# Kernel tuning notes

Measured on AMD Instinct MI355X. Metric: run time of the kernel, lower is better.

## Reference

```python
import jax, jax.numpy as jnp
import numpy as np

NEG = -1e30  # finite stand-in for -inf so logsumexp grads stay finite


def ctc_loss_mean(y_true, log_probs_tm, input_length, label_length, blank=0):
    """CTC loss (forward algorithm in log space), mean over batch.

    log_probs_tm: [T, B, C] time-major log-probabilities.
    y_true:       [B, L] dense int labels (blank=0 excluded from real labels).
    """
    T, B, C = log_probs_tm.shape
    L = y_true.shape[1]
    S = 2 * L + 1  # extended label length: blank, l1, blank, l2, ...
    ll = jnp.clip(label_length, 1, L)
    il = jnp.clip(input_length, 1, T)

    # Extended label sequence: blanks at even positions, labels at odd.
    ext = jnp.full((B, S), blank, dtype=jnp.int32).at[:, 1::2].set(y_true.astype(jnp.int32))
    ext_m2 = jnp.concatenate([jnp.full((B, 2), -1, jnp.int32), ext[:, :-2]], axis=1)
    # Skip transition (s-2 -> s) allowed only for label positions with no repeat.
    allow_skip = ((jnp.arange(S) % 2 == 1)[None, :]) & (ext != ext_m2)

    lp0 = jnp.take_along_axis(log_probs_tm[0], ext, axis=1)  # [B, S]
    alpha0 = jnp.full((B, S), NEG, log_probs_tm.dtype)
    alpha0 = alpha0.at[:, 0].set(lp0[:, 0]).at[:, 1].set(lp0[:, 1])

    def step(alpha, xs):
        lp_t, t = xs
        lpe = jnp.take_along_axis(lp_t, ext, axis=1)  # [B, S]
        a1 = jnp.concatenate([jnp.full((B, 1), NEG, alpha.dtype), alpha[:, :-1]], axis=1)
        a2 = jnp.concatenate([jnp.full((B, 2), NEG, alpha.dtype), alpha[:, :-2]], axis=1)
        a2 = jnp.where(allow_skip, a2, NEG)
        new = jax.nn.logsumexp(jnp.stack([alpha, a1, a2]), axis=0) + lpe
        # Freeze alpha once past each example's input_length.
        return jnp.where((t < il)[:, None], new, alpha), None

    alpha, _ = jax.lax.scan(step, alpha0, (log_probs_tm[1:], jnp.arange(1, T)))

    # Loss = -log(alpha[2*ll-1] + alpha[2*ll]) at the final (frozen) time step.
    idx = jnp.stack([2 * ll - 1, 2 * ll], axis=1)  # [B, 2]
    end_vals = jnp.take_along_axis(alpha, idx, axis=1)
    loss = -jax.nn.logsumexp(end_vals, axis=1)
    return jnp.mean(loss)


def setup_inputs() -> dict:
    key = jax.random.key(0)
    kx, kl, ki, kj = jax.random.split(key, 4)
    B, T, C, L = 64, 1024, 128, 256
    # y_pred are probabilities (module applies log), so softmax random logits.
    y_pred = jax.nn.softmax(jax.random.normal(kx, (B, T, C), jnp.float32), axis=-1)
    y_true = jax.random.randint(kl, (B, L), 1, C, jnp.int32)  # blank=0 excluded
    input_length = jax.random.randint(ki, (B,), T // 2, T + 1, jnp.int32)
    label_length = jax.random.randint(kj, (B,), L // 2, L + 1, jnp.int32)
    return {"y_true": y_true, "y_pred": y_pred,
            "input_length": input_length, "label_length": label_length}


def reference(y_true, y_pred, input_length, label_length):
    # Mirror CTCLayer.call: log + transpose to time-major, reshape lengths.
    log_tm = jnp.log(jnp.transpose(y_pred, (1, 0, 2)))  # [T, B, C]
    loss = ctc_loss_mean(y_true, log_tm,
                         input_length.reshape(-1), label_length.reshape(-1),
                         blank=0)
    return log_tm, loss
```

## Files before the change

### kernel.cpp

```cpp
#include <hip/hip_runtime.h>
#include <math.h>

constexpr int B = 64;
constexpr int T = 1024;
constexpr int C = 128;
constexpr int L = 256;
constexpr int S = 2 * L + 1;
constexpr int TRB = 2048;

template <int N> struct IC { static constexpr int value = N; };

__device__ __forceinline__ float shr1(float x) {
    return __int_as_float(__builtin_amdgcn_update_dpp(
        0, __float_as_int(x), 0x138 , 0xf, 0xf, false));
}

template <int CTRL>
__device__ __forceinline__ float maxdpp(float x) {
    float t = __int_as_float(__builtin_amdgcn_update_dpp(
        __float_as_int(x), __float_as_int(x), CTRL, 0xf, 0xf, false));
    return fmaxf(x, t);
}

__device__ __forceinline__ float wave_max_dpp(float x) {
    x = maxdpp<0x111>(x);
    x = maxdpp<0x112>(x);
    x = maxdpp<0x114>(x);
    x = maxdpp<0x118>(x);
    x = maxdpp<0x142>(x);
    x = maxdpp<0x143>(x);
    return __int_as_float(__builtin_amdgcn_readlane(__float_as_int(x), 63));
}

__global__
__attribute__((amdgpu_waves_per_eu(1, 1)))
__launch_bounds__(64)
void ctc_fused(
    const float* __restrict__ yp,
    const int*   __restrict__ yt,
    const int*   __restrict__ il_,
    const int*   __restrict__ ll_,
    float* __restrict__ out_log,
    float* __restrict__ out_loss)
{
    const int lane = threadIdx.x;
    if (blockIdx.x >= B) {
        int id = blockIdx.x - B;
        int bb = id >> 5;
        int ck = id & 31;
        const float4* src = (const float4*)yp + ((size_t)bb * T + ck * 32) * 32;
        float4* o4 = (float4*)out_log;
        #pragma unroll
        for (int k = 0; k < 16; ++k) {
            int o = k * 64 + lane;
            float4 v = src[o];
            int tt = ck * 32 + (o >> 5);
            int c4 = o & 31;
            float4 r;
            r.x = __logf(v.x); r.y = __logf(v.y);
            r.z = __logf(v.z); r.w = __logf(v.w);
            o4[((size_t)tt * B + bb) * 32 + c4] = r;
        }
        return;
    }

    const int b = blockIdx.x;

    __shared__ float lsh[2048];
    __shared__ float afin[S];

    int il = il_[b]; il = min(max(il, 1), T);
    int ll = ll_[b]; ll = min(max(ll, 1), L);
    const float* yb = yp + (size_t)b * T * C;

    int4 y4  = *(const int4*)(yt + b * L + 4 * lane);
    int  po  = lane ? 4 * lane - 4 : 0;
    int4 py4 = *(const int4*)(yt + b * L + po);
    int  ppw = yt[b * L + (lane >= 2 ? 4 * lane - 5 : 0)];

    int lab[8]   = {py4.x, py4.y, py4.z, py4.w, y4.x, y4.y, y4.z, y4.w};
    int labm1[8] = {ppw,   py4.x, py4.y, py4.z, py4.w, y4.x, y4.y, y4.z};
    float skf[8];
    #pragma unroll
    for (int k = 0; k < 8; ++k)
        skf[k] = ((4 * lane + k >= 5) && (lab[k] != labm1[k])) ? 1.f : 0.f;

    const int c0 = y4.x, c1 = y4.y, c2 = y4.z, c3 = y4.w;

    auto ldpair = [&](int m) -> float4 {
        int r = 2 * m + 1 + (lane >> 5);
        r = r > T - 1 ? T - 1 : r;
        return ((const float4*)(yb + (size_t)r * C))[lane & 31];
    };

    float p00 = yb[0];
    float p0l = yb[c0];

    float4 q0 = ldpair(0), q1 = ldpair(1);
    float4 q2 = ldpair(2), q3 = ldpair(3);
    float4 prr[8];
    #pragma unroll
    for (int m = 4; m <= 11; ++m) prr[m & 7] = ldpair(m);

    ((float4*)(lsh +   0))[lane] = q0;
    ((float4*)(lsh + 256))[lane] = q1;
    ((float4*)(lsh + 512))[lane] = q2;
    ((float4*)(lsh + 768))[lane] = q3;

    float gv[4][4][4], gbv[4][4];
    #pragma unroll
    for (int q = 0; q < 2; ++q)
        #pragma unroll
        for (int j = 0; j < 4; ++j) {
            const float* base = lsh + q * 512 + j * 128;
            gbv[q][j] = base[0];
            gv[q][j][0] = base[c0]; gv[q][j][1] = base[c1];
            gv[q][j][2] = base[c2]; gv[q][j][3] = base[c3];
        }

    float w[17];
    #pragma unroll
    for (int i = 0; i < 17; ++i) w[i] = 0.f;
    if (lane == 0) { w[8] = p00; w[9] = p0l; }

    auto halo = [&]() {
        #pragma unroll
        for (int k = 0; k < 8; ++k) w[k] = shr1(w[8 + k]);
    };
    halo();

    int lsi = 0;
    int t0 = 0;

    auto group = [&](auto Pc, auto S0c) {
        constexpr int P  = decltype(Pc)::value;
        constexpr int S0 = decltype(S0c)::value;
        constexpr int BF = (P + 2) & 3;
        float g1[4], g2[4], g3[4];
        #pragma unroll
        for (int j = 0; j < 4; ++j) {
            g1[j] = shr1(gv[P][j][1]);
            g2[j] = shr1(gv[P][j][2]);
            g3[j] = shr1(gv[P][j][3]);
        }
        #pragma unroll
        for (int j = 0; j < 4; ++j) {
            #pragma unroll
            for (int i = 16; i >= 2 * (j + 1); --i) {
                float acc = w[i] + w[i - 1];
                float g;
                if (i & 1) {
                    const int k = (i - 1) >> 1;
                    acc = fmaf(skf[k], w[i - 2], acc);
                    g = (k >= 4) ? gv[P][j][k - 4]
                                 : (k == 1 ? g1[j] : (k == 2 ? g2[j] : g3[j]));
                } else {
                    g = gbv[P][j];
                }
                w[i] = acc * g;
            }
        }
        ((float4*)(lsh + BF * 512      ))[lane] = prr[S0];
        ((float4*)(lsh + BF * 512 + 256))[lane] = prr[S0 + 1];
        prr[S0]     = ldpair((t0 >> 1) + 12);
        prr[S0 + 1] = ldpair((t0 >> 1) + 13);
        #pragma unroll
        for (int j = 0; j < 4; ++j) {
            const float* base = lsh + BF * 512 + j * 128;
            gbv[BF][j] = base[0];
            gv[BF][j][0] = base[c0]; gv[BF][j][1] = base[c1];
            gv[BF][j][2] = base[c2]; gv[BF][j][3] = base[c3];
        }
        __builtin_amdgcn_sched_barrier(0x7);
        halo();
        t0 += 4;
    };

    auto maxw = [&]() {
        return fmaxf(fmaxf(fmaxf(w[8], w[9]), fmaxf(w[10], w[11])),
                     fmaxf(fmaxf(w[12], w[13]),
                           fmaxf(fmaxf(w[14], w[15]), w[16])));
    };
    auto rescale = [&]() {
        float mm = wave_max_dpp(maxw());
        int eb = (__float_as_int(mm) >> 23) & 0xff;
        int sh = 350 - eb;
        sh = sh > 254 ? 254 : (sh < 1 ? 1 : sh);
        float inv = __int_as_float(sh << 23);
        #pragma unroll
        for (int i = 8; i < 17; ++i) w[i] *= inv;
        lsi -= sh - 127;
    };

    const int full_end = ((il - 1) >> 2) << 2;

    while (t0 + 16 <= full_end) {
        group(IC<0>{}, IC<4>{});
        group(IC<1>{}, IC<6>{});
        rescale();
        group(IC<2>{}, IC<0>{});
        group(IC<3>{}, IC<2>{});
        rescale();
    }

    if (t0 + 4 <= full_end) { group(IC<0>{}, IC<4>{}); rescale(); }
    if (t0 + 4 <= full_end) { group(IC<1>{}, IC<6>{}); rescale(); }
    if (t0 + 4 <= full_end) { group(IC<2>{}, IC<0>{}); }

    const int ph = (full_end >> 2) & 3;
    float tg[3][4], tb[3];
    switch (ph) {
    case 0:
        #pragma unroll
        for (int j = 0; j < 3; ++j) { tb[j]=gbv[0][j]; tg[j][0]=gv[0][j][0]; tg[j][1]=gv[0][j][1]; tg[j][2]=gv[0][j][2]; tg[j][3]=gv[0][j][3]; }
        break;
    case 1:
        #pragma unroll
        for (int j = 0; j < 3; ++j) { tb[j]=gbv[1][j]; tg[j][0]=gv[1][j][0]; tg[j][1]=gv[1][j][1]; tg[j][2]=gv[1][j][2]; tg[j][3]=gv[1][j][3]; }
        break;
    case 2:
        #pragma unroll
        for (int j = 0; j < 3; ++j) { tb[j]=gbv[2][j]; tg[j][0]=gv[2][j][0]; tg[j][1]=gv[2][j][1]; tg[j][2]=gv[2][j][2]; tg[j][3]=gv[2][j][3]; }
        break;
    default:
        #pragma unroll
        for (int j = 0; j < 3; ++j) { tb[j]=gbv[3][j]; tg[j][0]=gv[3][j][0]; tg[j][1]=gv[3][j][1]; tg[j][2]=gv[3][j][2]; tg[j][3]=gv[3][j][3]; }
        break;
    }
    #pragma unroll
    for (int j = 0; j < 3; ++j) {
        int r = full_end + 1 + j;
        if (r < il) {
            float hh = shr1(w[15]);
            float gb = tb[j];
            float n8  = (w[8] + hh) * gb;
            float n9  = fmaf(skf[4], hh,    w[9]  + w[8])  * tg[j][0];
            float n10 = (w[10] + w[9])  * gb;
            float n11 = fmaf(skf[5], w[9],  w[11] + w[10]) * tg[j][1];
            float n12 = (w[12] + w[11]) * gb;
            float n13 = fmaf(skf[6], w[11], w[13] + w[12]) * tg[j][2];
            float n14 = (w[14] + w[13]) * gb;
            float n15 = fmaf(skf[7], w[13], w[15] + w[14]) * tg[j][3];
            float n16 = (w[16] + w[15]) * gb;
            w[8] = n8;  w[9] = n9;  w[10] = n10; w[11] = n11; w[12] = n12;
            w[13] = n13; w[14] = n14; w[15] = n15; w[16] = n16;
        }
    }

    #pragma unroll
    for (int k = 0; k < 8; ++k) afin[8 * lane + k] = w[8 + k];
    if (lane == 63) afin[512] = w[16];
    __syncthreads();
    if (lane == 0) {
        float e1 = afin[2 * ll - 1];
        float e2 = afin[2 * ll];
        float sum = fmaxf(e1 + e2, 1e-37f);
        float loss = -(__log2f(sum) + (float)lsi) * 0.6931471805599453f;
        atomicAdd(out_loss, loss * (1.0f / (float)B));
    }
}

extern "C" void kernel_launch(void* const* d_in, const int* in_sizes, int n_in,
                              void* d_out, int out_size, void* d_ws, size_t ws_size,
                              hipStream_t stream) {
    const int*   y_true = (const int*)d_in[0];
    const float* y_pred = (const float*)d_in[1];
    const int*   in_len = (const int*)d_in[2];
    const int*   lb_len = (const int*)d_in[3];

    float* out_log  = (float*)d_out;
    float* out_loss = (float*)d_out + (size_t)T * B * C;

    hipMemsetAsync(out_loss, 0, sizeof(float), stream);
    ctc_fused<<<B + TRB, 64, 0, stream>>>(y_pred, y_true, in_len, lb_len,
                                          out_log, out_loss);
}
```

Baseline: 186.7 us.

## Gather emission probabilities directly from global memory and defer rescale application

Removes the LDS staging buffer and the float4 row prefetch; each group now gathers the needed per-label probabilities straight from global memory three groups ahead. The wave-wide max reduction for rescaling is split into a measure step and a later apply step, so the DPP reduction latency overlaps the next group's recurrence instead of stalling it. DPP moves use mov_dpp with bound_ctrl. The cost is scattered global loads, which may expose more latency than the LDS path did.

```diff
diff --git a/kernel.cpp b/kernel.cpp
--- a/kernel.cpp
+++ b/kernel.cpp
@@ -11,14 +11,24 @@
 template <int N> struct IC { static constexpr int value = N; };
 
 __device__ __forceinline__ float shr1(float x) {
+#if __has_builtin(__builtin_amdgcn_mov_dpp)
+    return __int_as_float(__builtin_amdgcn_mov_dpp(
+        __float_as_int(x), 0x138 , 0xf, 0xf, true));
+#else
     return __int_as_float(__builtin_amdgcn_update_dpp(
-        0, __float_as_int(x), 0x138 , 0xf, 0xf, false));
+        0, __float_as_int(x), 0x138, 0xf, 0xf, true));
+#endif
 }
 
 template <int CTRL>
 __device__ __forceinline__ float maxdpp(float x) {
+#if __has_builtin(__builtin_amdgcn_mov_dpp)
+    float t = __int_as_float(__builtin_amdgcn_mov_dpp(
+        __float_as_int(x), CTRL, 0xf, 0xf, true));
+#else
     float t = __int_as_float(__builtin_amdgcn_update_dpp(
-        __float_as_int(x), __float_as_int(x), CTRL, 0xf, 0xf, false));
+        0, __float_as_int(x), CTRL, 0xf, 0xf, true));
+#endif
     return fmaxf(x, t);
 }
 
@@ -66,7 +76,6 @@
 
     const int b = blockIdx.x;
 
-    __shared__ float lsh[2048];
     __shared__ float afin[S];
 
     int il = il_[b]; il = min(max(il, 1), T);
@@ -87,36 +96,31 @@
 
     const int c0 = y4.x, c1 = y4.y, c2 = y4.z, c3 = y4.w;
 
-    auto ldpair = [&](int m) -> float4 {
-        int r = 2 * m + 1 + (lane >> 5);
-        r = r > T - 1 ? T - 1 : r;
-        return ((const float4*)(yb + (size_t)r * C))[lane & 31];
+    int z0;
+    asm volatile("v_mov_b32 %0, 0" : "=v"(z0));
+
+    float gv[4][4][4], gbv[4][4];
+
+    auto fill = [&](auto Qc, int r0) {
+        constexpr int Q = decltype(Qc)::value;
+        #pragma unroll
+        for (int j = 0; j < 4; ++j) {
+            int r = r0 + j; r = r < T ? r : T - 1;
+            const float* rb = yb + (size_t)r * C;
+            gbv[Q][j]   = rb[z0];
+            gv[Q][j][0] = rb[c0];
+            gv[Q][j][1] = rb[c1];
+            gv[Q][j][2] = rb[c2];
+            gv[Q][j][3] = rb[c3];
+        }
     };
 
     float p00 = yb[0];
     float p0l = yb[c0];
 
-    float4 q0 = ldpair(0), q1 = ldpair(1);
-    float4 q2 = ldpair(2), q3 = ldpair(3);
-    float4 prr[8];
-    #pragma unroll
-    for (int m = 4; m <= 11; ++m) prr[m & 7] = ldpair(m);
-
-    ((float4*)(lsh +   0))[lane] = q0;
-    ((float4*)(lsh + 256))[lane] = q1;
-    ((float4*)(lsh + 512))[lane] = q2;
-    ((float4*)(lsh + 768))[lane] = q3;
-
-    float gv[4][4][4], gbv[4][4];
-    #pragma unroll
-    for (int q = 0; q < 2; ++q)
-        #pragma unroll
-        for (int j = 0; j < 4; ++j) {
-            const float* base = lsh + q * 512 + j * 128;
-            gbv[q][j] = base[0];
-            gv[q][j][0] = base[c0]; gv[q][j][1] = base[c1];
-            gv[q][j][2] = base[c2]; gv[q][j][3] = base[c3];
-        }
+    fill(IC<0>{}, 1);
+    fill(IC<1>{}, 5);
+    fill(IC<2>{}, 9);
 
     float w[17];
     #pragma unroll
@@ -132,10 +136,9 @@
     int lsi = 0;
     int t0 = 0;
 
-    auto group = [&](auto Pc, auto S0c) {
-        constexpr int P  = decltype(Pc)::value;
-        constexpr int S0 = decltype(S0c)::value;
-        constexpr int BF = (P + 2) & 3;
+    auto group = [&](auto Pc) {
+        constexpr int P = decltype(Pc)::value;
+        constexpr int F = (P + 3) & 3;
         float g1[4], g2[4], g3[4];
         #pragma unroll
         for (int j = 0; j < 4; ++j) {
@@ -160,17 +163,7 @@
                 w[i] = acc * g;
             }
         }
-        ((float4*)(lsh + BF * 512      ))[lane] = prr[S0];
-        ((float4*)(lsh + BF * 512 + 256))[lane] = prr[S0 + 1];
-        prr[S0]     = ldpair((t0 >> 1) + 12);
-        prr[S0 + 1] = ldpair((t0 >> 1) + 13);
-        #pragma unroll
-        for (int j = 0; j < 4; ++j) {
-            const float* base = lsh + BF * 512 + j * 128;
-            gbv[BF][j] = base[0];
-            gv[BF][j][0] = base[c0]; gv[BF][j][1] = base[c1];
-            gv[BF][j][2] = base[c2]; gv[BF][j][3] = base[c3];
-        }
+        fill(IC<F>{}, t0 + 13);
         __builtin_amdgcn_sched_barrier(0x7);
         halo();
         t0 += 4;
@@ -181,31 +174,42 @@
                      fmaxf(fmaxf(w[12], w[13]),
                            fmaxf(fmaxf(w[14], w[15]), w[16])));
     };
-    auto rescale = [&]() {
+
+    int pinv_bits = 127 << 23;
+    int psh = 0;
+    auto measure = [&]() {
         float mm = wave_max_dpp(maxw());
         int eb = (__float_as_int(mm) >> 23) & 0xff;
         int sh = 350 - eb;
         sh = sh > 254 ? 254 : (sh < 1 ? 1 : sh);
-        float inv = __int_as_float(sh << 23);
-        #pragma unroll
-        for (int i = 8; i < 17; ++i) w[i] *= inv;
-        lsi -= sh - 127;
-    };
+        pinv_bits = sh << 23;
+        psh = sh - 127;
+    };
+    auto apply = [&]() {
+        float inv = __int_as_float(pinv_bits);
+        #pragma unroll
+        for (int i = 0; i < 17; ++i) w[i] *= inv;
+        lsi -= psh;
+    };
+    auto rescale = [&]() { measure(); apply(); };
 
     const int full_end = ((il - 1) >> 2) << 2;
 
     while (t0 + 16 <= full_end) {
-        group(IC<0>{}, IC<4>{});
-        group(IC<1>{}, IC<6>{});
-        rescale();
-        group(IC<2>{}, IC<0>{});
-        group(IC<3>{}, IC<2>{});
-        rescale();
-    }
-
-    if (t0 + 4 <= full_end) { group(IC<0>{}, IC<4>{}); rescale(); }
-    if (t0 + 4 <= full_end) { group(IC<1>{}, IC<6>{}); rescale(); }
-    if (t0 + 4 <= full_end) { group(IC<2>{}, IC<0>{}); }
+        group(IC<0>{});
+        apply();
+        group(IC<1>{});
+        measure();
+        group(IC<2>{});
+        apply();
+        group(IC<3>{});
+        measure();
+    }
+    apply();
+
+    if (t0 + 4 <= full_end) { group(IC<0>{}); rescale(); }
+    if (t0 + 4 <= full_end) { group(IC<1>{}); rescale(); }
+    if (t0 + 4 <= full_end) { group(IC<2>{}); }
 
     const int ph = (full_end >> 2) & 3;
     float tg[3][4], tb[3];
```

Result: slower. 190.7 us (+2.1%).
